# Optimization experiments

Hardware: AMD Instinct MI355X
Metric: run time of the kernel (lower is better)

The kernel has to match this reference:

```python
import jax, jax.numpy as jnp
import numpy as np

DT = 0.1
THRESH = 10.0

def setup_inputs() -> dict:
    key = jax.random.key(0)
    ks = jax.random.split(key, 6)
    B, S, H, V = 2, 1024, 1024, 50257
    hidden_states = jax.random.normal(ks[0], (B, S, H), dtype=jnp.float32)
    ttu_state = jnp.zeros((B, 3), dtype=jnp.float32)
    W_imp = jax.random.normal(ks[1], (3, H), dtype=jnp.float32) * 0.02
    b_imp = jnp.zeros((3,), dtype=jnp.float32)
    W_lm = jax.random.normal(ks[2], (V, H), dtype=jnp.float32) * 0.02
    W_mod = jax.random.normal(ks[3], (V, 3), dtype=jnp.float32) * 0.02
    # gamma, alpha_c, beta_c, delta, alpha_d, epsilon, alpha_m
    ttu_params = jax.random.uniform(ks[4], (7,), dtype=jnp.float32, minval=0.1, maxval=1.0)
    return {"hidden_states": hidden_states, "ttu_state": ttu_state,
            "W_imp": W_imp, "b_imp": b_imp, "W_lm": W_lm, "W_mod": W_mod,
            "ttu_params": ttu_params}

def _ttu_scan(ttu_state, impulses, ttu_params):
    # impulses: [S, B, 3] (time-major for scan)
    gamma, alpha_c, beta_c, delta, alpha_d, epsilon, alpha_m = ttu_params
    def step(state, imp):
        phi_c, phi_d, phi_m = state[:, 0], state[:, 1], state[:, 2]
        dphi_c = gamma * imp[:, 0] - alpha_c * phi_c - beta_c * phi_c * phi_d
        dphi_d = delta * phi_c ** 2 - alpha_d * phi_d
        dphi_m = epsilon * phi_d - alpha_m * phi_m
        new_c = phi_c + DT * dphi_c
        new_d = phi_d + DT * dphi_d
        new_m = phi_m + DT * dphi_m
        # saturation damping on phi_d
        new_d = jnp.where(jnp.abs(new_d) > THRESH, jnp.float32(0.5), jnp.float32(1.0)) * new_d
        new_state = jnp.stack([new_c, new_d, new_m], axis=1)  # [B, 3]
        return new_state, new_state
    return jax.lax.scan(step, ttu_state, impulses)

def reference(hidden_states, ttu_state, W_imp, b_imp, W_lm, W_mod, ttu_params):
    # impulse projections computed in batch up front: [S, B, 3]
    impulses = jnp.einsum('bsh,dh->sbd', hidden_states, W_imp) + b_imp
    final_state, states = _ttu_scan(ttu_state, impulses, ttu_params)  # states: [S, B, 3]
    # base lm logits + 0.1 * modulation from ttu trajectory
    logits = jnp.einsum('bsh,vh->bsv', hidden_states, W_lm) \
           + 0.1 * jnp.einsum('sbd,vd->bsv', states, W_mod)
    return logits, final_state
```

## Files before the change

### kernel.cpp

```cpp
#include <hip/hip_runtime.h>
#include <hip/hip_bf16.h>

typedef float  f32x4  __attribute__((ext_vector_type(4)));
typedef short  bf16x8 __attribute__((ext_vector_type(8)));
typedef short  bf16x4 __attribute__((ext_vector_type(4)));

typedef const void __attribute__((address_space(1))) gv_t;
typedef void __attribute__((address_space(3))) sv_t;

namespace {

constexpr int B_ = 2;
constexpr int S_ = 1024;
constexpr int H_ = 1024;
constexpr int V_ = 50257;
constexpr int M_ = B_ * S_;
constexpr int VP1_ = 50304;
constexpr float DT_ = 0.1f;
constexpr float THRESH_ = 10.0f;

constexpr int BK = 64;
constexpr int NT = H_ / BK;

__device__ __forceinline__ unsigned short f2bf(float f) {
  union { float f; unsigned u; } x;
  x.f = f;
  x.u += 0x7FFFu + ((x.u >> 16) & 1u);
  return (unsigned short)(x.u >> 16);
}

__global__ void cvt_hidden_impulse_kernel(const float* __restrict__ hidden,
                                          const float* __restrict__ W_imp,
                                          const float* __restrict__ b_imp,
                                          unsigned short* __restrict__ hid_bf,
                                          float* __restrict__ imp) {
  const int m = blockIdx.x;
  const int t = threadIdx.x;
  const float4 hv = reinterpret_cast<const float4*>(hidden + (size_t)m * H_)[t];
  const float4 wv = reinterpret_cast<const float4*>(W_imp)[t];
  bf16x4 o;
  o[0] = (short)f2bf(hv.x); o[1] = (short)f2bf(hv.y);
  o[2] = (short)f2bf(hv.z); o[3] = (short)f2bf(hv.w);
  *(bf16x4*)(hid_bf + (size_t)m * H_ + t * 4) = o;
  float p = hv.x * wv.x + hv.y * wv.y + hv.z * wv.z + hv.w * wv.w;
  #pragma unroll
  for (int off = 32; off; off >>= 1) p += __shfl_down(p, off);
  __shared__ float partial[4];
  if ((t & 63) == 0) partial[t >> 6] = p;
  __syncthreads();
  if (t == 0) {
    const float v = partial[0] + partial[1] + partial[2] + partial[3] + b_imp[0];
    const int b = m >> 10;
    const int s = m & (S_ - 1);
    imp[s * B_ + b] = v;
  }
}

__device__ __forceinline__ void scan_body(const float* __restrict__ imp_s,
                                          const float* __restrict__ ttu_state,
                                          const float* __restrict__ ttu_params,
                                          float* __restrict__ states,
                                          float* __restrict__ final_out, int t) {
  if (t < B_) {
    const float gamma   = ttu_params[0];
    const float alpha_c = ttu_params[1];
    const float beta_c  = ttu_params[2];
    const float delta   = ttu_params[3];
    const float alpha_d = ttu_params[4];
    const float epsilon = ttu_params[5];
    const float alpha_m = ttu_params[6];
    float c = ttu_state[t * 3 + 0];
    float d = ttu_state[t * 3 + 1];
    float m = ttu_state[t * 3 + 2];
    for (int s = 0; s < S_; ++s) {
      const float ii = imp_s[s * B_ + t];
      const float dc = gamma * ii - alpha_c * c - beta_c * c * d;
      const float dd = delta * c * c - alpha_d * d;
      const float dm = epsilon * d - alpha_m * m;
      c = c + DT_ * dc;
      float nd = d + DT_ * dd;
      m = m + DT_ * dm;
      nd = (fabsf(nd) > THRESH_ ? 0.5f : 1.0f) * nd;
      d = nd;
      float* st = states + (size_t)(s * B_ + t) * 3;
      st[0] = c; st[1] = d; st[2] = m;
    }
    final_out[t * 3 + 0] = c;
    final_out[t * 3 + 1] = d;
    final_out[t * 3 + 2] = m;
  }
}

__global__ void ttu_scan_kernel(const float* __restrict__ imp,
                                const float* __restrict__ ttu_state,
                                const float* __restrict__ ttu_params,
                                float* __restrict__ states,
                                float* __restrict__ final_out) {
  __shared__ float imp_s[S_ * B_];
  const int t = threadIdx.x;
  for (int i = t; i < S_ * B_; i += 64) imp_s[i] = imp[i];
  __syncthreads();
  scan_body(imp_s, ttu_state, ttu_params, states, final_out, t);
}

__global__ void cvt_wlm_scan_kernel(const float* __restrict__ src,
                                    unsigned short* __restrict__ dst,
                                    long n_src, long n_dst,
                                    const float* __restrict__ imp,
                                    const float* __restrict__ ttu_state,
                                    const float* __restrict__ ttu_params,
                                    float* __restrict__ states,
                                    float* __restrict__ final_out) {
  __shared__ float imp_s[S_ * B_];
  const int t = threadIdx.x;
  if (blockIdx.x == gridDim.x - 1) {
    for (int i = t; i < S_ * B_; i += 256) imp_s[i] = imp[i];
    __syncthreads();
    scan_body(imp_s, ttu_state, ttu_params, states, final_out, t);
    return;
  }
  const long stride = (long)(gridDim.x - 1) * blockDim.x * 8;
  for (long i = ((long)blockIdx.x * blockDim.x + t) * 8; i < n_dst; i += stride) {
    bf16x8 v;
    if (i < n_src) {
      const float4 a = *(const float4*)(src + i);
      const float4 b = *(const float4*)(src + i + 4);
      v[0] = (short)f2bf(a.x); v[1] = (short)f2bf(a.y);
      v[2] = (short)f2bf(a.z); v[3] = (short)f2bf(a.w);
      v[4] = (short)f2bf(b.x); v[5] = (short)f2bf(b.y);
      v[6] = (short)f2bf(b.z); v[7] = (short)f2bf(b.w);
    } else {
      v = (bf16x8){0, 0, 0, 0, 0, 0, 0, 0};
    }
    *(bf16x8*)(dst + i) = v;
  }
}

__global__ __launch_bounds__(256, 2) void ttu_gemm_bf16_cnt_kernel(
    const unsigned short* __restrict__ Ab,
    const unsigned short* __restrict__ Bb,
    const float* __restrict__ states,
    const float* __restrict__ Wmod,
    float* __restrict__ out)
{
  __shared__ unsigned short AB_s[2][2][128 * BK];
  __shared__ float st_s[128][3];
  __shared__ float wm_s[128][3];

  const int t = threadIdx.x;
  const int cpx = gridDim.x >> 3;
  const int bid = (blockIdx.x & 7) * cpx + (blockIdx.x >> 3);
  const int mb = bid & 15;
  const int nb = bid >> 4;
  const int m0 = mb * 128;
  const int n0 = nb * 128;

  if (t < 128) {
    const int m = m0 + t;
    const int b = m >> 10;
    const int s = m & (S_ - 1);
    const float* st = states + (size_t)(s * B_ + b) * 3;
    st_s[t][0] = st[0]; st_s[t][1] = st[1]; st_s[t][2] = st[2];
  } else {
    const int tt = t - 128;
    const int n = n0 + tt;
    const bool ok = n < V_;
    wm_s[tt][0] = ok ? Wmod[n * 3 + 0] : 0.f;
    wm_s[tt][1] = ok ? Wmod[n * 3 + 1] : 0.f;
    wm_s[tt][2] = ok ? Wmod[n * 3 + 2] : 0.f;
  }

  const int lane = t & 63;
  const int wid  = t >> 6;
  const int lr   = lane >> 3;
  const int ch   = lane & 7;
  const int wm   = wid >> 1;
  const int wn   = wid & 1;
  const int lm   = lane & 15;
  const int kg   = lane >> 4;

  const unsigned short* Abase = Ab + (size_t)m0 * H_;
  const unsigned short* Bbase = Bb + (size_t)n0 * H_;
  const int r0 = wid * 32;

  auto STAGE = [&](unsigned short* As, unsigned short* Bs, int kt) {
    const int k0 = kt * BK;
    #pragma unroll
    for (int ins = 0; ins < 4; ++ins) {
      const int lrow = r0 + ins * 8 + lr;
      const int sch  = ch ^ (lrow & 7);
      __builtin_amdgcn_global_load_lds(
          (gv_t*)(Abase + (size_t)lrow * H_ + k0 + sch * 8),
          (sv_t*)(As + (r0 + ins * 8) * BK), 16, 0, 0);
    }
    #pragma unroll
    for (int ins = 0; ins < 4; ++ins) {
      const int lrow = r0 + ins * 8 + lr;
      const int sch  = ch ^ (lrow & 7);
      __builtin_amdgcn_global_load_lds(
          (gv_t*)(Bbase + (size_t)lrow * H_ + k0 + sch * 8),
          (sv_t*)(Bs + (r0 + ins * 8) * BK), 16, 0, 0);
    }
  };

  f32x4 acc[4][4];
  #pragma unroll
  for (int i = 0; i < 4; ++i)
    #pragma unroll
    for (int j = 0; j < 4; ++j)
      acc[i][j] = (f32x4){0.f, 0.f, 0.f, 0.f};

  unsigned short* Ac = &AB_s[0][0][0];
  unsigned short* Bc = &AB_s[0][1][0];
  unsigned short* An = &AB_s[1][0][0];
  unsigned short* Bn = &AB_s[1][1][0];

  STAGE(Ac, Bc, 0);

  for (int kt = 0; kt < NT; ++kt) {
    asm volatile("s_barrier" ::: "memory");
    if (kt + 1 < NT) {
      STAGE(An, Bn, kt + 1);
      asm volatile("s_waitcnt vmcnt(8)" ::: "memory");
    } else {
      asm volatile("s_waitcnt vmcnt(0)" ::: "memory");
    }
    asm volatile("s_barrier" ::: "memory");

    bf16x8 af[4][2], bfr[4][2];
    #pragma unroll
    for (int i = 0; i < 4; ++i) {
      const int arow = wm * 64 + i * 16 + lm;
      const int brow = wn * 64 + i * 16 + lm;
      #pragma unroll
      for (int ks = 0; ks < 2; ++ks) {
        af[i][ks]  = *(const bf16x8*)&Ac[arow * BK + (((ks * 4 + kg) ^ (arow & 7)) << 3)];
        bfr[i][ks] = *(const bf16x8*)&Bc[brow * BK + (((ks * 4 + kg) ^ (brow & 7)) << 3)];
      }
    }
    #pragma unroll
    for (int ks = 0; ks < 2; ++ks)
      #pragma unroll
      for (int i = 0; i < 4; ++i)
        #pragma unroll
        for (int j = 0; j < 4; ++j)
          acc[i][j] = __builtin_amdgcn_mfma_f32_16x16x32_bf16(af[i][ks], bfr[j][ks], acc[i][j], 0, 0, 0);

    unsigned short* tp;
    tp = Ac; Ac = An; An = tp;
    tp = Bc; Bc = Bn; Bn = tp;
  }

  #pragma unroll
  for (int i = 0; i < 4; ++i) {
    #pragma unroll
    for (int rr = 0; rr < 4; ++rr) {
      const int mloc = wm * 64 + i * 16 + kg * 4 + rr;
      const float s0 = st_s[mloc][0], s1 = st_s[mloc][1], s2 = st_s[mloc][2];
      float* orow = out + (size_t)(m0 + mloc) * V_ + n0;
      #pragma unroll
      for (int j = 0; j < 4; ++j) {
        const int nloc = wn * 64 + j * 16 + lm;
        if (n0 + nloc < V_) {
          const float corr = 0.1f * (s0 * wm_s[nloc][0] + s1 * wm_s[nloc][1] + s2 * wm_s[nloc][2]);
          __builtin_nontemporal_store(acc[i][j][rr] + corr, &orow[nloc]);
        }
      }
    }
  }
}

__global__ __launch_bounds__(256) void ttu_gemm_kernel(
    const float* __restrict__ Ag, const float* __restrict__ Bg,
    const float* __restrict__ states, const float* __restrict__ Wmod,
    float* __restrict__ out)
{
  __shared__ unsigned short A_s[128][40];
  __shared__ unsigned short B_s[128][40];
  __shared__ float st_s[128][3];
  __shared__ float wm_s[128][3];

  const int t   = threadIdx.x;
  const int bid = blockIdx.x;
  const int mb  = bid & 15;
  const int nb  = bid >> 4;
  const int m0  = mb * 128;
  const int n0  = nb * 128;

  if (t < 128) {
    const int m = m0 + t;
    const int b = m >> 10;
    const int s = m & (S_ - 1);
    const float* st = states + (size_t)(s * B_ + b) * 3;
    st_s[t][0] = st[0]; st_s[t][1] = st[1]; st_s[t][2] = st[2];
  } else {
    const int tt = t - 128;
    const int n  = n0 + tt;
    const bool ok = n < V_;
    wm_s[tt][0] = ok ? Wmod[n * 3 + 0] : 0.f;
    wm_s[tt][1] = ok ? Wmod[n * 3 + 1] : 0.f;
    wm_s[tt][2] = ok ? Wmod[n * 3 + 2] : 0.f;
  }

  const int r   = t >> 1;
  const int seg = t & 1;
  const float* arow = Ag + (size_t)(m0 + r) * H_ + seg * 16;
  const int  vrow = n0 + r;
  const bool bok  = vrow < V_;
  const float* brow = Bg + (size_t)(bok ? vrow : 0) * H_ + seg * 16;

  const int lane = t & 63;
  const int wid  = t >> 6;
  const int wm   = wid >> 1;
  const int wn   = wid & 1;
  const int lm   = lane & 15;
  const int kg   = lane >> 4;

  f32x4 acc[4][4];
  #pragma unroll
  for (int i = 0; i < 4; ++i)
    #pragma unroll
    for (int j = 0; j < 4; ++j)
      acc[i][j] = (f32x4){0.f, 0.f, 0.f, 0.f};

  for (int kt = 0; kt < H_ / 32; ++kt) {
    const int k0 = kt * 32;
    const float4 av0 = *(const float4*)(arow + k0 + 0);
    const float4 av1 = *(const float4*)(arow + k0 + 4);
    const float4 av2 = *(const float4*)(arow + k0 + 8);
    const float4 av3 = *(const float4*)(arow + k0 + 12);
    float4 bv0 = {0,0,0,0}, bv1 = {0,0,0,0}, bv2 = {0,0,0,0}, bv3 = {0,0,0,0};
    if (bok) {
      bv0 = *(const float4*)(brow + k0 + 0);
      bv1 = *(const float4*)(brow + k0 + 4);
      bv2 = *(const float4*)(brow + k0 + 8);
      bv3 = *(const float4*)(brow + k0 + 12);
    }
    __syncthreads();
    #define CVT4(v) (bf16x4){(short)f2bf((v).x), (short)f2bf((v).y), (short)f2bf((v).z), (short)f2bf((v).w)}
    *(bf16x4*)&A_s[r][seg * 16 + 0]  = CVT4(av0);
    *(bf16x4*)&A_s[r][seg * 16 + 4]  = CVT4(av1);
    *(bf16x4*)&A_s[r][seg * 16 + 8]  = CVT4(av2);
    *(bf16x4*)&A_s[r][seg * 16 + 12] = CVT4(av3);
    *(bf16x4*)&B_s[r][seg * 16 + 0]  = CVT4(bv0);
    *(bf16x4*)&B_s[r][seg * 16 + 4]  = CVT4(bv1);
    *(bf16x4*)&B_s[r][seg * 16 + 8]  = CVT4(bv2);
    *(bf16x4*)&B_s[r][seg * 16 + 12] = CVT4(bv3);
    #undef CVT4
    __syncthreads();
    bf16x8 af[4], bf[4];
    #pragma unroll
    for (int i = 0; i < 4; ++i) {
      af[i] = *(const bf16x8*)&A_s[wm * 64 + i * 16 + lm][kg * 8];
      bf[i] = *(const bf16x8*)&B_s[wn * 64 + i * 16 + lm][kg * 8];
    }
    #pragma unroll
    for (int i = 0; i < 4; ++i)
      #pragma unroll
      for (int j = 0; j < 4; ++j)
        acc[i][j] = __builtin_amdgcn_mfma_f32_16x16x32_bf16(af[i], bf[j], acc[i][j], 0, 0, 0);
  }

  #pragma unroll
  for (int i = 0; i < 4; ++i) {
    #pragma unroll
    for (int rr = 0; rr < 4; ++rr) {
      const int mloc = wm * 64 + i * 16 + kg * 4 + rr;
      const float s0 = st_s[mloc][0], s1 = st_s[mloc][1], s2 = st_s[mloc][2];
      float* orow = out + (size_t)(m0 + mloc) * V_ + n0;
      #pragma unroll
      for (int j = 0; j < 4; ++j) {
        const int nloc = wn * 64 + j * 16 + lm;
        if (n0 + nloc < V_) {
          const float corr = 0.1f * (s0 * wm_s[nloc][0] + s1 * wm_s[nloc][1] + s2 * wm_s[nloc][2]);
          orow[nloc] = acc[i][j][rr] + corr;
        }
      }
    }
  }
}

}

extern "C" void kernel_launch(void* const* d_in, const int* in_sizes, int n_in,
                              void* d_out, int out_size, void* d_ws, size_t ws_size,
                              hipStream_t stream) {
  const float* hidden     = (const float*)d_in[0];
  const float* ttu_state  = (const float*)d_in[1];
  const float* W_imp      = (const float*)d_in[2];
  const float* b_imp      = (const float*)d_in[3];
  const float* W_lm       = (const float*)d_in[4];
  const float* W_mod      = (const float*)d_in[5];
  const float* ttu_params = (const float*)d_in[6];
  float* out = (float*)d_out;

  float* imp    = (float*)d_ws;
  float* states = imp + S_ * B_;
  float* final_out = out + (size_t)B_ * S_ * V_;

  const size_t need = 32768 + (size_t)M_ * H_ * 2 + (size_t)VP1_ * H_ * 2;

  if (ws_size >= need) {
    unsigned short* hid_bf = (unsigned short*)((char*)d_ws + 32768);
    unsigned short* wlm_bf = hid_bf + (size_t)M_ * H_;
    cvt_hidden_impulse_kernel<<<M_, 256, 0, stream>>>(hidden, W_imp, b_imp, hid_bf, imp);
    cvt_wlm_scan_kernel<<<2049, 256, 0, stream>>>(W_lm, wlm_bf,
                                                  (long)V_ * H_, (long)VP1_ * H_,
                                                  imp, ttu_state, ttu_params,
                                                  states, final_out);
    const int grid = (VP1_ / 128) * (M_ / 128);
    ttu_gemm_bf16_cnt_kernel<<<grid, 256, 0, stream>>>(hid_bf, wlm_bf, states, W_mod, out);
  } else {
    cvt_hidden_impulse_kernel<<<M_, 256, 0, stream>>>(hidden, W_imp, b_imp,
                                                      (unsigned short*)d_ws, imp);
    ttu_scan_kernel<<<1, 64, 0, stream>>>(imp, ttu_state, ttu_params, states, final_out);
    const int grid = ((V_ + 127) / 128) * (M_ / 128);
    ttu_gemm_kernel<<<grid, 256, 0, stream>>>(hidden, W_lm, states, W_mod, out);
  }
}
```

Measured before the change: 527.4 us.

## Switch bf16 GEMM to BK=32 triple-buffered pipeline with three blocks per CU

The main GEMM kernel now uses a K tile of 32 instead of 64 and a three-stage LDS ring buffer, prefetching two tiles ahead. The swizzle and load mapping are rebuilt for the narrower rows, and occupancy is raised to three blocks per CU. The goal is to hide global-load latency better and raise occupancy, at the cost of twice as many barrier iterations. The output stores also change from nontemporal to regular stores.

```diff
diff --git a/kernel.cpp b/kernel.cpp
--- a/kernel.cpp
+++ b/kernel.cpp
@@ -19,8 +19,8 @@
 constexpr float DT_ = 0.1f;
 constexpr float THRESH_ = 10.0f;
 
-constexpr int BK = 64;
-constexpr int NT = H_ / BK;
+constexpr int BK3 = 32;
+constexpr int NT3 = H_ / BK3;
 
 __device__ __forceinline__ unsigned short f2bf(float f) {
   union { float f; unsigned u; } x;
@@ -136,14 +136,15 @@
   }
 }
 
-__global__ __launch_bounds__(256, 2) void ttu_gemm_bf16_cnt_kernel(
+__global__ __launch_bounds__(256, 3) void ttu_gemm_bf16_128x32_kernel(
     const unsigned short* __restrict__ Ab,
     const unsigned short* __restrict__ Bb,
     const float* __restrict__ states,
     const float* __restrict__ Wmod,
     float* __restrict__ out)
 {
-  __shared__ unsigned short AB_s[2][2][128 * BK];
+  __shared__ unsigned short A_s[3][128 * BK3];
+  __shared__ unsigned short B_s[3][128 * BK3];
   __shared__ float st_s[128][3];
   __shared__ float wm_s[128][3];
 
@@ -172,8 +173,8 @@
 
   const int lane = t & 63;
   const int wid  = t >> 6;
-  const int lr   = lane >> 3;
-  const int ch   = lane & 7;
+  const int lr   = lane >> 2;
+  const int ch   = lane & 3;
   const int wm   = wid >> 1;
   const int wn   = wid & 1;
   const int lm   = lane & 15;
@@ -181,25 +182,22 @@
 
   const unsigned short* Abase = Ab + (size_t)m0 * H_;
   const unsigned short* Bbase = Bb + (size_t)n0 * H_;
-  const int r0 = wid * 32;
-
-  auto STAGE = [&](unsigned short* As, unsigned short* Bs, int kt) {
-    const int k0 = kt * BK;
-    #pragma unroll
-    for (int ins = 0; ins < 4; ++ins) {
-      const int lrow = r0 + ins * 8 + lr;
-      const int sch  = ch ^ (lrow & 7);
-      __builtin_amdgcn_global_load_lds(
-          (gv_t*)(Abase + (size_t)lrow * H_ + k0 + sch * 8),
-          (sv_t*)(As + (r0 + ins * 8) * BK), 16, 0, 0);
-    }
-    #pragma unroll
-    for (int ins = 0; ins < 4; ++ins) {
-      const int lrow = r0 + ins * 8 + lr;
-      const int sch  = ch ^ (lrow & 7);
-      __builtin_amdgcn_global_load_lds(
-          (gv_t*)(Bbase + (size_t)lrow * H_ + k0 + sch * 8),
-          (sv_t*)(Bs + (r0 + ins * 8) * BK), 16, 0, 0);
+
+  auto STAGE = [&](int buf, int kt) {
+    const int k0 = kt * BK3;
+    #pragma unroll
+    for (int h = 0; h < 2; ++h) {
+      const unsigned short* gb = h ? Bbase : Abase;
+      unsigned short* ls = h ? &B_s[buf][0] : &A_s[buf][0];
+      #pragma unroll
+      for (int n = 0; n < 2; ++n) {
+        const int rbase = wid * 32 + n * 16;
+        const int r  = rbase + lr;
+        const int sc = ch ^ ((r >> 1) & 3);
+        __builtin_amdgcn_global_load_lds(
+            (gv_t*)(gb + (size_t)r * H_ + k0 + sc * 8),
+            (sv_t*)(ls + rbase * BK3), 16, 0, 0);
+      }
     }
   };
 
@@ -210,45 +208,41 @@
     for (int j = 0; j < 4; ++j)
       acc[i][j] = (f32x4){0.f, 0.f, 0.f, 0.f};
 
-  unsigned short* Ac = &AB_s[0][0][0];
-  unsigned short* Bc = &AB_s[0][1][0];
-  unsigned short* An = &AB_s[1][0][0];
-  unsigned short* Bn = &AB_s[1][1][0];
-
-  STAGE(Ac, Bc, 0);
-
-  for (int kt = 0; kt < NT; ++kt) {
+  STAGE(0, 0);
+  STAGE(1, 1);
+
+  int cur = 0, nxt2 = 2;
+  for (int kt = 0; kt < NT3; ++kt) {
     asm volatile("s_barrier" ::: "memory");
-    if (kt + 1 < NT) {
-      STAGE(An, Bn, kt + 1);
+    if (kt + 2 < NT3) {
+      STAGE(nxt2, kt + 2);
       asm volatile("s_waitcnt vmcnt(8)" ::: "memory");
+    } else if (kt + 1 < NT3) {
+      asm volatile("s_waitcnt vmcnt(4)" ::: "memory");
     } else {
       asm volatile("s_waitcnt vmcnt(0)" ::: "memory");
     }
     asm volatile("s_barrier" ::: "memory");
 
-    bf16x8 af[4][2], bfr[4][2];
+    const unsigned short* As = &A_s[cur][0];
+    const unsigned short* Bs = &B_s[cur][0];
+
+    bf16x8 af[4], bfr[4];
     #pragma unroll
     for (int i = 0; i < 4; ++i) {
       const int arow = wm * 64 + i * 16 + lm;
       const int brow = wn * 64 + i * 16 + lm;
+      af[i]  = *(const bf16x8*)&As[arow * BK3 + ((kg ^ ((arow >> 1) & 3)) << 3)];
+      bfr[i] = *(const bf16x8*)&Bs[brow * BK3 + ((kg ^ ((brow >> 1) & 3)) << 3)];
+    }
+    #pragma unroll
+    for (int i = 0; i < 4; ++i)
       #pragma unroll
-      for (int ks = 0; ks < 2; ++ks) {
-        af[i][ks]  = *(const bf16x8*)&Ac[arow * BK + (((ks * 4 + kg) ^ (arow & 7)) << 3)];
-        bfr[i][ks] = *(const bf16x8*)&Bc[brow * BK + (((ks * 4 + kg) ^ (brow & 7)) << 3)];
-      }
-    }
-    #pragma unroll
-    for (int ks = 0; ks < 2; ++ks)
-      #pragma unroll
-      for (int i = 0; i < 4; ++i)
-        #pragma unroll
-        for (int j = 0; j < 4; ++j)
-          acc[i][j] = __builtin_amdgcn_mfma_f32_16x16x32_bf16(af[i][ks], bfr[j][ks], acc[i][j], 0, 0, 0);
-
-    unsigned short* tp;
-    tp = Ac; Ac = An; An = tp;
-    tp = Bc; Bc = Bn; Bn = tp;
+      for (int j = 0; j < 4; ++j)
+        acc[i][j] = __builtin_amdgcn_mfma_f32_16x16x32_bf16(af[i], bfr[j], acc[i][j], 0, 0, 0);
+
+    cur = (cur == 2) ? 0 : cur + 1;
+    nxt2 = (nxt2 == 2) ? 0 : nxt2 + 1;
   }
 
   #pragma unroll
@@ -263,7 +257,7 @@
         const int nloc = wn * 64 + j * 16 + lm;
         if (n0 + nloc < V_) {
           const float corr = 0.1f * (s0 * wm_s[nloc][0] + s1 * wm_s[nloc][1] + s2 * wm_s[nloc][2]);
-          __builtin_nontemporal_store(acc[i][j][rr] + corr, &orow[nloc]);
+          orow[nloc] = acc[i][j][rr] + corr;
         }
       }
     }
@@ -409,7 +403,7 @@
                                                   imp, ttu_state, ttu_params,
                                                   states, final_out);
     const int grid = (VP1_ / 128) * (M_ / 128);
-    ttu_gemm_bf16_cnt_kernel<<<grid, 256, 0, stream>>>(hid_bf, wlm_bf, states, W_mod, out);
+    ttu_gemm_bf16_128x32_kernel<<<grid, 256, 0, stream>>>(hid_bf, wlm_bf, states, W_mod, out);
   } else {
     cvt_hidden_impulse_kernel<<<M_, 256, 0, stream>>>(hidden, W_imp, b_imp,
                                                       (unsigned short*)d_ws, imp);
```

New measurement: 487.9 us. 1.08x faster.

## Load A operand directly from global into registers, stage only B in LDS

Applied to the files above, without the earlier changes.

The GEMM kernel stops staging the A (hidden) tile through LDS. Each wave now loads its A fragments straight from global memory into registers, while only the B tile is double-buffered in LDS. This halves LDS footprint, so the occupancy hint rises to 3 blocks per CU, and the hand-tuned vmcnt/s_barrier scheme is replaced with __syncthreads. The A reads become uncoalesced 16-byte per-lane global loads with no prefetch ahead of the MFMAs, and each A row is re-read by both wn waves. Output stores also switch from nontemporal to regular stores.

```diff
diff --git a/kernel.cpp b/kernel.cpp
--- a/kernel.cpp
+++ b/kernel.cpp
@@ -136,14 +136,14 @@
   }
 }
 
-__global__ __launch_bounds__(256, 2) void ttu_gemm_bf16_cnt_kernel(
+__global__ __launch_bounds__(256, 3) void ttu_gemm_bf16_adirect_kernel(
     const unsigned short* __restrict__ Ab,
     const unsigned short* __restrict__ Bb,
     const float* __restrict__ states,
     const float* __restrict__ Wmod,
     float* __restrict__ out)
 {
-  __shared__ unsigned short AB_s[2][2][128 * BK];
+  __shared__ unsigned short B_s[2][128 * BK];
   __shared__ float st_s[128][3];
   __shared__ float wm_s[128][3];
 
@@ -179,20 +179,12 @@
   const int lm   = lane & 15;
   const int kg   = lane >> 4;
 
-  const unsigned short* Abase = Ab + (size_t)m0 * H_;
   const unsigned short* Bbase = Bb + (size_t)n0 * H_;
+  const unsigned short* Aln = Ab + (size_t)(m0 + wm * 64 + lm) * H_ + kg * 8;
   const int r0 = wid * 32;
 
-  auto STAGE = [&](unsigned short* As, unsigned short* Bs, int kt) {
+  auto STAGE_B = [&](unsigned short* Bs, int kt) {
     const int k0 = kt * BK;
-    #pragma unroll
-    for (int ins = 0; ins < 4; ++ins) {
-      const int lrow = r0 + ins * 8 + lr;
-      const int sch  = ch ^ (lrow & 7);
-      __builtin_amdgcn_global_load_lds(
-          (gv_t*)(Abase + (size_t)lrow * H_ + k0 + sch * 8),
-          (sv_t*)(As + (r0 + ins * 8) * BK), 16, 0, 0);
-    }
     #pragma unroll
     for (int ins = 0; ins < 4; ++ins) {
       const int lrow = r0 + ins * 8 + lr;
@@ -210,33 +202,29 @@
     for (int j = 0; j < 4; ++j)
       acc[i][j] = (f32x4){0.f, 0.f, 0.f, 0.f};
 
-  unsigned short* Ac = &AB_s[0][0][0];
-  unsigned short* Bc = &AB_s[0][1][0];
-  unsigned short* An = &AB_s[1][0][0];
-  unsigned short* Bn = &AB_s[1][1][0];
-
-  STAGE(Ac, Bc, 0);
+  unsigned short* Bc = &B_s[0][0];
+  unsigned short* Bn = &B_s[1][0];
+
+  STAGE_B(Bc, 0);
+  __syncthreads();
 
   for (int kt = 0; kt < NT; ++kt) {
-    asm volatile("s_barrier" ::: "memory");
-    if (kt + 1 < NT) {
-      STAGE(An, Bn, kt + 1);
-      asm volatile("s_waitcnt vmcnt(8)" ::: "memory");
-    } else {
-      asm volatile("s_waitcnt vmcnt(0)" ::: "memory");
-    }
-    asm volatile("s_barrier" ::: "memory");
-
-    bf16x8 af[4][2], bfr[4][2];
-    #pragma unroll
-    for (int i = 0; i < 4; ++i) {
-      const int arow = wm * 64 + i * 16 + lm;
-      const int brow = wn * 64 + i * 16 + lm;
-      #pragma unroll
-      for (int ks = 0; ks < 2; ++ks) {
-        af[i][ks]  = *(const bf16x8*)&Ac[arow * BK + (((ks * 4 + kg) ^ (arow & 7)) << 3)];
-        bfr[i][ks] = *(const bf16x8*)&Bc[brow * BK + (((ks * 4 + kg) ^ (brow & 7)) << 3)];
-      }
+    if (kt + 1 < NT) STAGE_B(Bn, kt + 1);
+
+    bf16x8 af[4][2];
+    #pragma unroll
+    for (int i = 0; i < 4; ++i)
+      #pragma unroll
+      for (int ks = 0; ks < 2; ++ks)
+        af[i][ks] = *(const bf16x8*)(Aln + (size_t)(i * 16) * H_ + kt * BK + ks * 32);
+
+    bf16x8 bfr[4][2];
+    #pragma unroll
+    for (int j = 0; j < 4; ++j) {
+      const int brow = wn * 64 + j * 16 + lm;
+      #pragma unroll
+      for (int ks = 0; ks < 2; ++ks)
+        bfr[j][ks] = *(const bf16x8*)&Bc[brow * BK + (((ks * 4 + kg) ^ (brow & 7)) << 3)];
     }
     #pragma unroll
     for (int ks = 0; ks < 2; ++ks)
@@ -246,9 +234,8 @@
         for (int j = 0; j < 4; ++j)
           acc[i][j] = __builtin_amdgcn_mfma_f32_16x16x32_bf16(af[i][ks], bfr[j][ks], acc[i][j], 0, 0, 0);
 
-    unsigned short* tp;
-    tp = Ac; Ac = An; An = tp;
-    tp = Bc; Bc = Bn; Bn = tp;
+    __syncthreads();
+    unsigned short* tp = Bc; Bc = Bn; Bn = tp;
   }
 
   #pragma unroll
@@ -263,7 +250,7 @@
         const int nloc = wn * 64 + j * 16 + lm;
         if (n0 + nloc < V_) {
           const float corr = 0.1f * (s0 * wm_s[nloc][0] + s1 * wm_s[nloc][1] + s2 * wm_s[nloc][2]);
-          __builtin_nontemporal_store(acc[i][j][rr] + corr, &orow[nloc]);
+          orow[nloc] = acc[i][j][rr] + corr;
         }
       }
     }
@@ -409,7 +396,7 @@
                                                   imp, ttu_state, ttu_params,
                                                   states, final_out);
     const int grid = (VP1_ / 128) * (M_ / 128);
-    ttu_gemm_bf16_cnt_kernel<<<grid, 256, 0, stream>>>(hid_bf, wlm_bf, states, W_mod, out);
+    ttu_gemm_bf16_adirect_kernel<<<grid, 256, 0, stream>>>(hid_bf, wlm_bf, states, W_mod, out);
   } else {
     cvt_hidden_impulse_kernel<<<M_, 256, 0, stream>>>(hidden, W_imp, b_imp,
                                                       (unsigned short*)d_ws, imp);
```

Result: slower. 623.0 us (+18.1%).

## Enlarge bf16 GEMM tile to 256x256 with 32x32 MFMA and 8 waves

Applied to the files above, without the earlier changes.

Replaces the 128x128, 4-wave bf16 GEMM with a 256x256 tile computed by 8 waves using 32x32x16 MFMA instructions. A-fragment loads are double-buffered across M sub-tiles, and s_setprio is raised around the MFMA bursts. The padded vocab grows to a multiple of 256. The goal is higher arithmetic intensity and fewer LDS reads per FLOP. In exchange it uses 128KB of LDS for double buffering, which likely limits occupancy to one block per CU. It also wastes more work on padded columns and switches from nontemporal to regular stores.

```diff
diff --git a/kernel.cpp b/kernel.cpp
--- a/kernel.cpp
+++ b/kernel.cpp
@@ -2,6 +2,7 @@
 #include <hip/hip_bf16.h>
 
 typedef float  f32x4  __attribute__((ext_vector_type(4)));
+typedef float  f32x16 __attribute__((ext_vector_type(16)));
 typedef short  bf16x8 __attribute__((ext_vector_type(8)));
 typedef short  bf16x4 __attribute__((ext_vector_type(4)));
 
@@ -15,7 +16,7 @@
 constexpr int H_ = 1024;
 constexpr int V_ = 50257;
 constexpr int M_ = B_ * S_;
-constexpr int VP1_ = 50304;
+constexpr int VP2_ = 50432;
 constexpr float DT_ = 0.1f;
 constexpr float THRESH_ = 10.0f;
 
@@ -136,33 +137,34 @@
   }
 }
 
-__global__ __launch_bounds__(256, 2) void ttu_gemm_bf16_cnt_kernel(
+__global__ __launch_bounds__(512, 2) void ttu_gemm_bf16_256w_kernel(
     const unsigned short* __restrict__ Ab,
     const unsigned short* __restrict__ Bb,
     const float* __restrict__ states,
     const float* __restrict__ Wmod,
     float* __restrict__ out)
 {
-  __shared__ unsigned short AB_s[2][2][128 * BK];
-  __shared__ float st_s[128][3];
-  __shared__ float wm_s[128][3];
+  __shared__ unsigned short A_s[2][256 * BK];
+  __shared__ unsigned short B_s[2][256 * BK];
+  __shared__ float st_s[256][3];
+  __shared__ float wm_s[256][3];
 
   const int t = threadIdx.x;
   const int cpx = gridDim.x >> 3;
   const int bid = (blockIdx.x & 7) * cpx + (blockIdx.x >> 3);
-  const int mb = bid & 15;
-  const int nb = bid >> 4;
-  const int m0 = mb * 128;
-  const int n0 = nb * 128;
-
-  if (t < 128) {
+  const int mb = bid & 7;
+  const int nb = bid >> 3;
+  const int m0 = mb * 256;
+  const int n0 = nb * 256;
+
+  if (t < 256) {
     const int m = m0 + t;
     const int b = m >> 10;
     const int s = m & (S_ - 1);
     const float* st = states + (size_t)(s * B_ + b) * 3;
     st_s[t][0] = st[0]; st_s[t][1] = st[1]; st_s[t][2] = st[2];
   } else {
-    const int tt = t - 128;
+    const int tt = t - 256;
     const int n = n0 + tt;
     const bool ok = n < V_;
     wm_s[tt][0] = ok ? Wmod[n * 3 + 0] : 0.f;
@@ -174,96 +176,106 @@
   const int wid  = t >> 6;
   const int lr   = lane >> 3;
   const int ch   = lane & 7;
-  const int wm   = wid >> 1;
-  const int wn   = wid & 1;
-  const int lm   = lane & 15;
-  const int kg   = lane >> 4;
+  const int wmi  = wid >> 2;
+  const int wni  = wid & 3;
+  const int l31  = lane & 31;
+  const int kh   = lane >> 5;
 
   const unsigned short* Abase = Ab + (size_t)m0 * H_;
   const unsigned short* Bbase = Bb + (size_t)n0 * H_;
-  const int r0 = wid * 32;
-
-  auto STAGE = [&](unsigned short* As, unsigned short* Bs, int kt) {
+
+  auto STAGE_ALL = [&](int buf, int kt) {
     const int k0 = kt * BK;
     #pragma unroll
-    for (int ins = 0; ins < 4; ++ins) {
-      const int lrow = r0 + ins * 8 + lr;
-      const int sch  = ch ^ (lrow & 7);
-      __builtin_amdgcn_global_load_lds(
-          (gv_t*)(Abase + (size_t)lrow * H_ + k0 + sch * 8),
-          (sv_t*)(As + (r0 + ins * 8) * BK), 16, 0, 0);
-    }
-    #pragma unroll
-    for (int ins = 0; ins < 4; ++ins) {
-      const int lrow = r0 + ins * 8 + lr;
-      const int sch  = ch ^ (lrow & 7);
-      __builtin_amdgcn_global_load_lds(
-          (gv_t*)(Bbase + (size_t)lrow * H_ + k0 + sch * 8),
-          (sv_t*)(Bs + (r0 + ins * 8) * BK), 16, 0, 0);
+    for (int h = 0; h < 4; ++h) {
+      const unsigned short* gb = (h < 2) ? Abase : Bbase;
+      unsigned short* ls = (h < 2) ? &A_s[buf][0] : &B_s[buf][0];
+      const int half = (h & 1) * 128;
+      #pragma unroll
+      for (int n = 0; n < 2; ++n) {
+        const int rbase = half + wid * 16 + n * 8;
+        const int r  = rbase + lr;
+        const int sc = ch ^ (r & 7);
+        __builtin_amdgcn_global_load_lds(
+            (gv_t*)(gb + (size_t)r * H_ + k0 + sc * 8),
+            (sv_t*)(ls + rbase * BK), 16, 0, 0);
+      }
     }
   };
 
-  f32x4 acc[4][4];
+  f32x16 acc[4][2];
   #pragma unroll
   for (int i = 0; i < 4; ++i)
     #pragma unroll
-    for (int j = 0; j < 4; ++j)
-      acc[i][j] = (f32x4){0.f, 0.f, 0.f, 0.f};
-
-  unsigned short* Ac = &AB_s[0][0][0];
-  unsigned short* Bc = &AB_s[0][1][0];
-  unsigned short* An = &AB_s[1][0][0];
-  unsigned short* Bn = &AB_s[1][1][0];
-
-  STAGE(Ac, Bc, 0);
-
+    for (int j = 0; j < 2; ++j)
+      acc[i][j] = (f32x16){0.f,0.f,0.f,0.f,0.f,0.f,0.f,0.f,
+                           0.f,0.f,0.f,0.f,0.f,0.f,0.f,0.f};
+
+  STAGE_ALL(0, 0);
+
+  int cur = 0;
   for (int kt = 0; kt < NT; ++kt) {
+    const int nxt = cur ^ 1;
     asm volatile("s_barrier" ::: "memory");
     if (kt + 1 < NT) {
-      STAGE(An, Bn, kt + 1);
+      STAGE_ALL(nxt, kt + 1);
       asm volatile("s_waitcnt vmcnt(8)" ::: "memory");
     } else {
       asm volatile("s_waitcnt vmcnt(0)" ::: "memory");
     }
     asm volatile("s_barrier" ::: "memory");
 
-    bf16x8 af[4][2], bfr[4][2];
-    #pragma unroll
-    for (int i = 0; i < 4; ++i) {
-      const int arow = wm * 64 + i * 16 + lm;
-      const int brow = wn * 64 + i * 16 + lm;
-      #pragma unroll
-      for (int ks = 0; ks < 2; ++ks) {
-        af[i][ks]  = *(const bf16x8*)&Ac[arow * BK + (((ks * 4 + kg) ^ (arow & 7)) << 3)];
-        bfr[i][ks] = *(const bf16x8*)&Bc[brow * BK + (((ks * 4 + kg) ^ (brow & 7)) << 3)];
+    const unsigned short* As = &A_s[cur][0];
+    const unsigned short* Bs = &B_s[cur][0];
+
+    bf16x8 bfr[2][4];
+    #pragma unroll
+    for (int nf = 0; nf < 2; ++nf) {
+      const int r = wni * 64 + nf * 32 + l31;
+      #pragma unroll
+      for (int ks = 0; ks < 4; ++ks)
+        bfr[nf][ks] = *(const bf16x8*)&Bs[r * BK + (((ks * 2 + kh) ^ (r & 7)) << 3)];
+    }
+    bf16x8 af[2][4];
+    {
+      const int r = wmi * 128 + l31;
+      #pragma unroll
+      for (int ks = 0; ks < 4; ++ks)
+        af[0][ks] = *(const bf16x8*)&As[r * BK + (((ks * 2 + kh) ^ (r & 7)) << 3)];
+    }
+    #pragma unroll
+    for (int mf = 0; mf < 4; ++mf) {
+      if (mf < 3) {
+        const int r = wmi * 128 + (mf + 1) * 32 + l31;
+        #pragma unroll
+        for (int ks = 0; ks < 4; ++ks)
+          af[(mf + 1) & 1][ks] = *(const bf16x8*)&As[r * BK + (((ks * 2 + kh) ^ (r & 7)) << 3)];
       }
-    }
-    #pragma unroll
-    for (int ks = 0; ks < 2; ++ks)
-      #pragma unroll
-      for (int i = 0; i < 4; ++i)
+      __builtin_amdgcn_s_setprio(1);
+      #pragma unroll
+      for (int ks = 0; ks < 4; ++ks)
         #pragma unroll
-        for (int j = 0; j < 4; ++j)
-          acc[i][j] = __builtin_amdgcn_mfma_f32_16x16x32_bf16(af[i][ks], bfr[j][ks], acc[i][j], 0, 0, 0);
-
-    unsigned short* tp;
-    tp = Ac; Ac = An; An = tp;
-    tp = Bc; Bc = Bn; Bn = tp;
+        for (int nf = 0; nf < 2; ++nf)
+          acc[mf][nf] = __builtin_amdgcn_mfma_f32_32x32x16_bf16(
+              af[mf & 1][ks], bfr[nf][ks], acc[mf][nf], 0, 0, 0);
+      __builtin_amdgcn_s_setprio(0);
+    }
+    cur ^= 1;
   }
 
   #pragma unroll
-  for (int i = 0; i < 4; ++i) {
-    #pragma unroll
-    for (int rr = 0; rr < 4; ++rr) {
-      const int mloc = wm * 64 + i * 16 + kg * 4 + rr;
+  for (int mf = 0; mf < 4; ++mf) {
+    #pragma unroll
+    for (int r = 0; r < 16; ++r) {
+      const int mloc = wmi * 128 + mf * 32 + (r & 3) + 8 * (r >> 2) + 4 * kh;
       const float s0 = st_s[mloc][0], s1 = st_s[mloc][1], s2 = st_s[mloc][2];
       float* orow = out + (size_t)(m0 + mloc) * V_ + n0;
       #pragma unroll
-      for (int j = 0; j < 4; ++j) {
-        const int nloc = wn * 64 + j * 16 + lm;
+      for (int nf = 0; nf < 2; ++nf) {
+        const int nloc = wni * 64 + nf * 32 + l31;
         if (n0 + nloc < V_) {
           const float corr = 0.1f * (s0 * wm_s[nloc][0] + s1 * wm_s[nloc][1] + s2 * wm_s[nloc][2]);
-          __builtin_nontemporal_store(acc[i][j][rr] + corr, &orow[nloc]);
+          orow[nloc] = acc[mf][nf][r] + corr;
         }
       }
     }
@@ -398,18 +410,18 @@
   float* states = imp + S_ * B_;
   float* final_out = out + (size_t)B_ * S_ * V_;
 
-  const size_t need = 32768 + (size_t)M_ * H_ * 2 + (size_t)VP1_ * H_ * 2;
+  const size_t need = 32768 + (size_t)M_ * H_ * 2 + (size_t)VP2_ * H_ * 2;
 
   if (ws_size >= need) {
     unsigned short* hid_bf = (unsigned short*)((char*)d_ws + 32768);
     unsigned short* wlm_bf = hid_bf + (size_t)M_ * H_;
     cvt_hidden_impulse_kernel<<<M_, 256, 0, stream>>>(hidden, W_imp, b_imp, hid_bf, imp);
     cvt_wlm_scan_kernel<<<2049, 256, 0, stream>>>(W_lm, wlm_bf,
-                                                  (long)V_ * H_, (long)VP1_ * H_,
+                                                  (long)V_ * H_, (long)VP2_ * H_,
                                                   imp, ttu_state, ttu_params,
                                                   states, final_out);
-    const int grid = (VP1_ / 128) * (M_ / 128);
-    ttu_gemm_bf16_cnt_kernel<<<grid, 256, 0, stream>>>(hid_bf, wlm_bf, states, W_mod, out);
+    const int grid = (VP2_ / 256) * (M_ / 256);
+    ttu_gemm_bf16_256w_kernel<<<grid, 512, 0, stream>>>(hid_bf, wlm_bf, states, W_mod, out);
   } else {
     cvt_hidden_impulse_kernel<<<M_, 256, 0, stream>>>(hidden, W_imp, b_imp,
                                                       (unsigned short*)d_ws, imp);
```

Result: faster. 493.4 us (-6.4%).
